# Performance work log

Measured on AMD Instinct MI355X. Metric: run time of the kernel, lower is better.

The kernel has to match this reference:

```python
import jax, jax.numpy as jnp
import numpy as np

NEG_SLOPE = 0.2  # DenseGATConv default negative_slope


def _add_self_loops(adj):
    n = adj.shape[-1]
    idx = jnp.arange(n)
    return adj.at[:, idx, idx].set(1.0)


def dense_gat_conv(x, adj, W, att_src, att_dst, bias, concat):
    """PyG DenseGATConv forward (eval mode, add_loop=True).
    x: [B,N,F], adj: [B,N,N] (0/1), W: [F,H*C], att_*: [H,C], bias: [H*C] or [C]."""
    B, N, _ = x.shape
    H, C = att_src.shape
    h = (x @ W).reshape(B, N, H, C)                     # projected features
    a_src = jnp.einsum('bnhc,hc->bnh', h, att_src)      # [B,N,H]
    a_dst = jnp.einsum('bnhc,hc->bnh', h, att_dst)      # [B,N,H]
    # alpha[b,i,j,h] = a_src[b,j,h] + a_dst[b,i,h]
    alpha = a_src[:, None, :, :] + a_dst[:, :, None, :]  # [B,N,N,H]
    alpha = jax.nn.leaky_relu(alpha, NEG_SLOPE)
    adj = _add_self_loops(adj)
    alpha = jnp.where(adj[..., None] == 0, -jnp.inf, alpha)
    alpha = jax.nn.softmax(alpha, axis=2)               # softmax over sources j
    out = jnp.einsum('bijh,bjhc->bihc', alpha, h)       # [B,N,H,C]
    out = out.reshape(B, N, H * C) if concat else out.mean(axis=2)
    return out + bias


def setup_inputs() -> dict:
    key = jax.random.key(0)
    ks = jax.random.split(key, 10)
    B, N, F, H, C, NC = 1, 4096, 512, 8, 64, 16
    x = jax.random.normal(ks[0], (B, N, F), dtype=jnp.float32)
    adj = (jax.random.uniform(ks[1], (B, N, N)) < 0.01).astype(jnp.float32)
    s1 = 1.0 / np.sqrt(F)
    s2 = 1.0 / np.sqrt(H * C)
    return {
        'x': x,
        'adj': adj,
        'W1': jax.random.normal(ks[2], (F, H * C), dtype=jnp.float32) * s1,
        'att_src1': jax.random.normal(ks[3], (H, C), dtype=jnp.float32) * s1,
        'att_dst1': jax.random.normal(ks[4], (H, C), dtype=jnp.float32) * s1,
        'b1': jnp.zeros((H * C,), dtype=jnp.float32),
        'W2': jax.random.normal(ks[5], (H * C, NC), dtype=jnp.float32) * s2,
        'att_src2': jax.random.normal(ks[6], (1, NC), dtype=jnp.float32) * s2,
        'att_dst2': jax.random.normal(ks[7], (1, NC), dtype=jnp.float32) * s2,
        'b2': jnp.zeros((NC,), dtype=jnp.float32),
    }


def reference(x, adj, W1, att_src1, att_dst1, b1, W2, att_src2, att_dst2, b2):
    # eval mode: all dropout(p=0.6) layers are identity
    h = dense_gat_conv(x, adj, W1, att_src1, att_dst1, b1, concat=True)
    h = jax.nn.elu(h)
    out = dense_gat_conv(h, adj, W2, att_src2, att_dst2, b2, concat=False)
    return out
```

## Files before the change

kernel.cpp:

```cpp
#include <hip/hip_runtime.h>
#include <hip/hip_bf16.h>
#include <hip/hip_fp16.h>

#define N_NODES 4096
#define F_IN    512
#define HC      512
#define H_HEADS 8
#define C_DIM   64
#define NCLS    16
#define CAP     192
#define NEG_SLOPE 0.2f

typedef __bf16 bf16x8 __attribute__((ext_vector_type(8)));
typedef float  f32x4  __attribute__((ext_vector_type(4)));
typedef unsigned short us8 __attribute__((ext_vector_type(8)));


#define XBLKS 1024
#define WBLKS 64

__global__ __launch_bounds__(256) void k_prep(const float* __restrict__ x,
                                              const float* __restrict__ W,
                                              const float* __restrict__ adj,
                                              ushort* __restrict__ xhi,
                                              ushort* __restrict__ xlo,
                                              ushort* __restrict__ whiT,
                                              ushort* __restrict__ wloT,
                                              int* __restrict__ row_cnt,
                                              int* __restrict__ col_idx) {
    __shared__ float tile[64][65];
    __shared__ int cnt_s;
    int b = blockIdx.x;
    int t = threadIdx.x;
    if (b < XBLKS) {
        int tid = b * 256 + t;
        int rg = tid >> 9;
        rg = tid >> 10;
        int c  = tid & 1023;
        int kb = c >> 6;
        int l  = c & 63;
        int row = rg * 16 + (l & 15);
        int kbase = kb * 32 + (l >> 4) * 8;
        const float* src = &x[(size_t)row * F_IN + kbase];
        float4 v0 = *(const float4*)&src[0];
        float4 v1 = *(const float4*)&src[4];
        float f[8] = {v0.x, v0.y, v0.z, v0.w, v1.x, v1.y, v1.z, v1.w};
        us8 hv, lv;
#pragma unroll
        for (int u = 0; u < 8; ++u) {
            __bf16 h = (__bf16)f[u];
            __bf16 lo_ = (__bf16)(f[u] - (float)h);
            hv[u] = __builtin_bit_cast(unsigned short, h);
            lv[u] = __builtin_bit_cast(unsigned short, lo_);
        }
        *(us8*)&xhi[(size_t)tid * 8] = hv;
        *(us8*)&xlo[(size_t)tid * 8] = lv;
    } else if (b < XBLKS + WBLKS) {
        int bb = b - XBLKS;
        int n0 = (bb & 7) * 64, k0 = (bb >> 3) * 64;
#pragma unroll
        for (int i = 0; i < 4; ++i) {
            int r = i * 16 + (t >> 4);
            int c = (t & 15) * 4;
            *(float4*)&tile[r][c] = *(const float4*)&W[(size_t)(k0 + r) * HC + n0 + c];
        }
        __syncthreads();
        int rg_local = t >> 6;
        int l = t & 63;
        int n_local = rg_local * 16 + (l & 15);
#pragma unroll
        for (int kb_local = 0; kb_local < 2; ++kb_local) {
            int k_local = kb_local * 32 + (l >> 4) * 8;
            us8 hv, lv;
#pragma unroll
            for (int u = 0; u < 8; ++u) {
                float f = tile[k_local + u][n_local];
                __bf16 h = (__bf16)f;
                __bf16 lo_ = (__bf16)(f - (float)h);
                hv[u] = __builtin_bit_cast(unsigned short, h);
                lv[u] = __builtin_bit_cast(unsigned short, lo_);
            }
            int rg = (n0 >> 4) + rg_local;
            int kb = (k0 >> 5) + kb_local;
            size_t off = ((size_t)(rg * 16 + kb) * 64 + l) * 8;
            *(us8*)&whiT[off] = hv;
            *(us8*)&wloT[off] = lv;
        }
    } else {
        int i = b - (XBLKS + WBLKS);
        if (t == 0) cnt_s = 0;
        __syncthreads();
        const float4* row = (const float4*)(adj + (size_t)i * N_NODES);
        int* cols = col_idx + (size_t)i * CAP;
#pragma unroll
        for (int it = 0; it < 4; ++it) {
            int idx4 = it * 256 + t;
            float4 v = row[idx4];
            int j0 = idx4 * 4;
            if (v.x != 0.f && j0 + 0 != i) { int p = atomicAdd(&cnt_s, 1); if (p < CAP - 1) cols[p] = j0 + 0; }
            if (v.y != 0.f && j0 + 1 != i) { int p = atomicAdd(&cnt_s, 1); if (p < CAP - 1) cols[p] = j0 + 1; }
            if (v.z != 0.f && j0 + 2 != i) { int p = atomicAdd(&cnt_s, 1); if (p < CAP - 1) cols[p] = j0 + 2; }
            if (v.w != 0.f && j0 + 3 != i) { int p = atomicAdd(&cnt_s, 1); if (p < CAP - 1) cols[p] = j0 + 3; }
        }
        __syncthreads();
        if (t == 0) {
            int p = min(cnt_s, CAP - 1);
            cols[p] = i;
            row_cnt[i] = p + 1;
        }
    }
}

__global__ __launch_bounds__(256) void k_gemm1(const ushort* __restrict__ Ahi,
                                               const ushort* __restrict__ Alo,
                                               const ushort* __restrict__ Bhi,
                                               const ushort* __restrict__ Blo,
                                               const float* __restrict__ att_src,
                                               const float* __restrict__ att_dst,
                                               __half* __restrict__ C,
                                               float* __restrict__ a_src,
                                               float* __restrict__ a_dst) {
    __shared__ __align__(16) ushort smem[4][2048];
    __shared__ float s_s[2][64], s_d[2][64];
    int t = threadIdx.x;
    int w = t >> 6, lane = t & 63;
    int n0 = blockIdx.x * 64;
    int m0 = blockIdx.y * 64;
    const ushort* src = (w == 0) ? Ahi : (w == 1) ? Alo : (w == 2) ? Bhi : Blo;
    int rg0 = ((w < 2) ? m0 : n0) >> 4;
    int mw = (w & 1) * 32, nw = (w >> 1) * 32;
    f32x4 acc[2][2] = {};
    for (int kb = 0; kb < 16; ++kb) {
#pragma unroll
        for (int g = 0; g < 4; ++g) {
            const ushort* gp = src + ((size_t)((rg0 + g) * 16 + kb) * 64 + lane) * 8;
            __builtin_amdgcn_global_load_lds(
                (const __attribute__((address_space(1))) void*)gp,
                (__attribute__((address_space(3))) void*)&smem[w][g * 512],
                16, 0, 0);
        }
        __syncthreads();
        bf16x8 ahi[2], alo[2], bhi[2], blo[2];
#pragma unroll
        for (int mi = 0; mi < 2; ++mi) {
            int g = (mw >> 4) + mi;
            ahi[mi] = __builtin_bit_cast(bf16x8, *(const us8*)&smem[0][g * 512 + lane * 8]);
            alo[mi] = __builtin_bit_cast(bf16x8, *(const us8*)&smem[1][g * 512 + lane * 8]);
        }
#pragma unroll
        for (int ni = 0; ni < 2; ++ni) {
            int g = (nw >> 4) + ni;
            bhi[ni] = __builtin_bit_cast(bf16x8, *(const us8*)&smem[2][g * 512 + lane * 8]);
            blo[ni] = __builtin_bit_cast(bf16x8, *(const us8*)&smem[3][g * 512 + lane * 8]);
        }
#pragma unroll
        for (int mi = 0; mi < 2; ++mi)
#pragma unroll
            for (int ni = 0; ni < 2; ++ni) {
                acc[mi][ni] = __builtin_amdgcn_mfma_f32_16x16x32_bf16(ahi[mi], bhi[ni], acc[mi][ni], 0, 0, 0);
                acc[mi][ni] = __builtin_amdgcn_mfma_f32_16x16x32_bf16(alo[mi], bhi[ni], acc[mi][ni], 0, 0, 0);
                acc[mi][ni] = __builtin_amdgcn_mfma_f32_16x16x32_bf16(ahi[mi], blo[ni], acc[mi][ni], 0, 0, 0);
            }
        __syncthreads();
    }
    int r0 = (lane >> 4) * 4;
    int cn = lane & 15;
    float as0 = att_src[n0 + nw + cn],      as1 = att_src[n0 + nw + 16 + cn];
    float ad0 = att_dst[n0 + nw + cn],      ad1 = att_dst[n0 + nw + 16 + cn];
#pragma unroll
    for (int mi = 0; mi < 2; ++mi)
#pragma unroll
        for (int r = 0; r < 4; ++r) {
            float ps = acc[mi][0][r] * as0 + acc[mi][1][r] * as1;
            float pd = acc[mi][0][r] * ad0 + acc[mi][1][r] * ad1;
#pragma unroll
            for (int o = 1; o < 16; o <<= 1) {
                ps += __shfl_xor(ps, o, 64);
                pd += __shfl_xor(pd, o, 64);
            }
            if (cn == 0) {
                int row = mw + mi * 16 + r0 + r;
                s_s[w >> 1][row] = ps;
                s_d[w >> 1][row] = pd;
            }
        }
#pragma unroll
    for (int mi = 0; mi < 2; ++mi)
#pragma unroll
        for (int ni = 0; ni < 2; ++ni) {
            size_t base = (size_t)(m0 + mw + mi * 16 + r0) * HC + (n0 + nw + ni * 16 + cn);
#pragma unroll
            for (int r = 0; r < 4; ++r)
                C[base + (size_t)r * HC] = __float2half(acc[mi][ni][r]);
        }
    __syncthreads();
    if (t < 64) {
        a_src[(m0 + t) * H_HEADS + blockIdx.x] = s_s[0][t] + s_s[1][t];
        a_dst[(m0 + t) * H_HEADS + blockIdx.x] = s_d[0][t] + s_d[1][t];
    }
}

__global__ __launch_bounds__(256) void k_agg1(const __half* __restrict__ hf,
                                              const float* __restrict__ a_src,
                                              const float* __restrict__ a_dst,
                                              const int* __restrict__ row_cnt,
                                              const int* __restrict__ col_idx,
                                              const float* __restrict__ b1,
                                              __half* __restrict__ elu1) {
    int i = blockIdx.x;
    int t = threadIdx.x;
    __shared__ float wL[CAP][H_HEADS];
    __shared__ int   colL[CAP];
    __shared__ float denom[H_HEADS];
    __shared__ float ad[H_HEADS];
    int cnt = row_cnt[i];
    if (t < H_HEADS) ad[t] = a_dst[i * H_HEADS + t];
    for (int j = t; j < cnt; j += 256) colL[j] = col_idx[(size_t)i * CAP + j];
    __syncthreads();
    for (int idx = t; idx < cnt * H_HEADS; idx += 256) {
        int j = idx >> 3, h = idx & 7;
        float l = a_src[colL[j] * H_HEADS + h] + ad[h];
        l = (l > 0.f) ? l : NEG_SLOPE * l;
        wL[j][h] = __expf(l);
    }
    __syncthreads();
    {
        int h = t >> 5, l32 = t & 31;
        float s = 0.f;
        for (int j = l32; j < cnt; j += 32) s += wL[j][h];
#pragma unroll
        for (int o = 16; o > 0; o >>= 1) s += __shfl_down(s, o, 32);
        if (l32 == 0) denom[h] = s;
    }
    __syncthreads();
    int e = t * 2;
    int h = e >> 6;
    float ax = 0.f, ay = 0.f;
    int j = 0;
    for (; j + 4 <= cnt; j += 4) {
        int c0 = colL[j], c1 = colL[j + 1], c2 = colL[j + 2], c3 = colL[j + 3];
        float2 v0 = __half22float2(*(const __half2*)&hf[(size_t)c0 * HC + e]);
        float2 v1 = __half22float2(*(const __half2*)&hf[(size_t)c1 * HC + e]);
        float2 v2 = __half22float2(*(const __half2*)&hf[(size_t)c2 * HC + e]);
        float2 v3 = __half22float2(*(const __half2*)&hf[(size_t)c3 * HC + e]);
        float w0 = wL[j][h], w1 = wL[j + 1][h], w2 = wL[j + 2][h], w3 = wL[j + 3][h];
        ax += w0 * v0.x + w1 * v1.x + w2 * v2.x + w3 * v3.x;
        ay += w0 * v0.y + w1 * v1.y + w2 * v2.y + w3 * v3.y;
    }
    for (; j < cnt; ++j) {
        int c0 = colL[j];
        float2 v0 = __half22float2(*(const __half2*)&hf[(size_t)c0 * HC + e]);
        float w0 = wL[j][h];
        ax += w0 * v0.x;
        ay += w0 * v0.y;
    }
    float inv = 1.f / denom[h];
    float o0 = ax * inv + b1[e];
    float o1 = ay * inv + b1[e + 1];
    o0 = (o0 > 0.f) ? o0 : (__expf(o0) - 1.f);
    o1 = (o1 > 0.f) ? o1 : (__expf(o1) - 1.f);
    *(__half2*)&elu1[(size_t)i * HC + e] = __floats2half2_rn(o0, o1);
}

__global__ __launch_bounds__(256) void k_gemm2(const __half* __restrict__ elu1,
                                               const float* __restrict__ W2,
                                               const float* __restrict__ att_src2,
                                               const float* __restrict__ att_dst2,
                                               float* __restrict__ h2,
                                               float* __restrict__ a_src2,
                                               float* __restrict__ a_dst2) {
    __shared__ float W2s[HC * NCLS];
    __shared__ float h2s[16][NCLS];
    int t = threadIdx.x;
    int n0 = blockIdx.x * 16;
#pragma unroll
    for (int u = 0; u < 8; ++u) {
        int idx = (u * 256 + t) * 4;
        *(float4*)&W2s[idx] = *(const float4*)&W2[idx];
    }
    __syncthreads();
    int nl = t >> 4, c = t & 15;
    const __half2* row = (const __half2*)(elu1 + (size_t)(n0 + nl) * HC);
    float acc = 0.f;
    for (int k = 0; k < HC; k += 4) {
        float2 v0 = __half22float2(row[k >> 1]);
        float2 v1 = __half22float2(row[(k >> 1) + 1]);
        acc += v0.x * W2s[(k + 0) * NCLS + c] + v0.y * W2s[(k + 1) * NCLS + c]
             + v1.x * W2s[(k + 2) * NCLS + c] + v1.y * W2s[(k + 3) * NCLS + c];
    }
    h2[(size_t)(n0 + nl) * NCLS + c] = acc;
    h2s[nl][c] = acc;
    __syncthreads();
    if (t < 16) {
        float s = 0.f, d = 0.f;
#pragma unroll
        for (int cc = 0; cc < NCLS; ++cc) {
            s += h2s[t][cc] * att_src2[cc];
            d += h2s[t][cc] * att_dst2[cc];
        }
        a_src2[n0 + t] = s;
        a_dst2[n0 + t] = d;
    }
}

__global__ __launch_bounds__(256) void k_agg2(const float* __restrict__ h2,
                                              const float* __restrict__ a_src2,
                                              const float* __restrict__ a_dst2,
                                              const int* __restrict__ row_cnt,
                                              const int* __restrict__ col_idx,
                                              const float* __restrict__ b2,
                                              float* __restrict__ out) {
    int t = threadIdx.x;
    int w = t >> 6, lane = t & 63;
    int i = blockIdx.x * 4 + w;
    __shared__ float ew[4][CAP];
    __shared__ int   colL[4][CAP];
    int cnt = row_cnt[i];
    float adi = a_dst2[i];
    float sum = 0.f;
    for (int j = lane; j < cnt; j += 64) {
        int col = col_idx[(size_t)i * CAP + j];
        colL[w][j] = col;
        float l = a_src2[col] + adi;
        l = (l > 0.f) ? l : NEG_SLOPE * l;
        float e = __expf(l);
        ew[w][j] = e;
        sum += e;
    }
#pragma unroll
    for (int o = 32; o > 0; o >>= 1) sum += __shfl_xor(sum, o, 64);
    int q = lane >> 4, c = lane & 15;
    float acc = 0.f;
    for (int j = q; j < cnt; j += 4)
        acc += ew[w][j] * h2[(size_t)colL[w][j] * NCLS + c];
    acc += __shfl_down(acc, 32, 64);
    acc += __shfl_down(acc, 16, 64);
    if (lane < NCLS)
        out[(size_t)i * NCLS + lane] = acc / sum + b2[lane];
}

extern "C" void kernel_launch(void* const* d_in, const int* in_sizes, int n_in,
                              void* d_out, int out_size, void* d_ws, size_t ws_size,
                              hipStream_t stream) {
    const float* x        = (const float*)d_in[0];
    const float* adj      = (const float*)d_in[1];
    const float* W1       = (const float*)d_in[2];
    const float* att_src1 = (const float*)d_in[3];
    const float* att_dst1 = (const float*)d_in[4];
    const float* b1       = (const float*)d_in[5];
    const float* W2       = (const float*)d_in[6];
    const float* att_src2 = (const float*)d_in[7];
    const float* att_dst2 = (const float*)d_in[8];
    const float* b2       = (const float*)d_in[9];
    float* out = (float*)d_out;

    char* ws = (char*)d_ws;
    int*    row_cnt = (int*)ws;     ws += (size_t)N_NODES * 4;
    int*    col_idx = (int*)ws;     ws += (size_t)N_NODES * CAP * 4;
    __half* h1f     = (__half*)ws;  ws += (size_t)N_NODES * HC * 2;
    float*  a_src   = (float*)ws;   ws += (size_t)N_NODES * H_HEADS * 4;
    float*  a_dst   = (float*)ws;   ws += (size_t)N_NODES * H_HEADS * 4;
    __half* elu1    = (__half*)ws;  ws += (size_t)N_NODES * HC * 2;
    float*  h2      = (float*)ws;   ws += (size_t)N_NODES * NCLS * 4;
    float*  as2     = (float*)ws;   ws += (size_t)N_NODES * 4;
    float*  ad2     = (float*)ws;   ws += (size_t)N_NODES * 4;
    ushort* x_hi    = (ushort*)ws;  ws += (size_t)N_NODES * F_IN * 2;
    ushort* x_lo    = (ushort*)ws;  ws += (size_t)N_NODES * F_IN * 2;
    ushort* w_hiT   = (ushort*)ws;  ws += (size_t)F_IN * HC * 2;
    ushort* w_loT   = (ushort*)ws;  ws += (size_t)F_IN * HC * 2;

    hipLaunchKernelGGL(k_prep, dim3(XBLKS + WBLKS + N_NODES), dim3(256), 0, stream,
                       x, W1, adj, x_hi, x_lo, w_hiT, w_loT, row_cnt, col_idx);
    hipLaunchKernelGGL(k_gemm1, dim3(HC / 64, N_NODES / 64), dim3(256), 0, stream,
                       x_hi, x_lo, w_hiT, w_loT, att_src1, att_dst1, h1f, a_src, a_dst);
    hipLaunchKernelGGL(k_agg1, dim3(N_NODES), dim3(256), 0, stream,
                       h1f, a_src, a_dst, row_cnt, col_idx, b1, elu1);
    hipLaunchKernelGGL(k_gemm2, dim3(N_NODES / 16), dim3(256), 0, stream,
                       elu1, W2, att_src2, att_dst2, h2, as2, ad2);
    hipLaunchKernelGGL(k_agg2, dim3(N_NODES / 4), dim3(256), 0, stream,
                       h2, as2, ad2, row_cnt, col_idx, b2, out);
}
```

Measured before the change: 165.2 us.

## Fuse second-layer projection into layer-1 aggregation kernel

The layer-1 aggregation kernel now keeps each row's ELU output in shared memory and immediately multiplies it by W2, also computing the layer-2 attention scores. This removes the separate gemm2 launch and the fp16 ELU intermediate's write and re-read. The cost is that every one of 4096 blocks reloads the full 32 KB W2 into shared memory, and the larger shared footprint may reduce occupancy. It also adds extra block barriers and a serial tail per row.

```diff
diff --git a/kernel.cpp b/kernel.cpp
--- a/kernel.cpp
+++ b/kernel.cpp
@@ -34,8 +34,7 @@
     int t = threadIdx.x;
     if (b < XBLKS) {
         int tid = b * 256 + t;
-        int rg = tid >> 9;
-        rg = tid >> 10;
+        int rg = tid >> 10;
         int c  = tid & 1023;
         int kb = c >> 6;
         int l  = c & 63;
@@ -206,16 +205,30 @@
                                               const int* __restrict__ row_cnt,
                                               const int* __restrict__ col_idx,
                                               const float* __restrict__ b1,
-                                              __half* __restrict__ elu1) {
+                                              const float* __restrict__ W2,
+                                              const float* __restrict__ att_src2,
+                                              const float* __restrict__ att_dst2,
+                                              float* __restrict__ h2,
+                                              float* __restrict__ a_src2,
+                                              float* __restrict__ a_dst2) {
     int i = blockIdx.x;
     int t = threadIdx.x;
     __shared__ float wL[CAP][H_HEADS];
     __shared__ int   colL[CAP];
     __shared__ float denom[H_HEADS];
     __shared__ float ad[H_HEADS];
+    __shared__ float W2s[HC * NCLS];
+    __shared__ float elu_s[HC];
+    __shared__ float part[16][NCLS + 1];
+    __shared__ float h2row[NCLS];
     int cnt = row_cnt[i];
     if (t < H_HEADS) ad[t] = a_dst[i * H_HEADS + t];
     for (int j = t; j < cnt; j += 256) colL[j] = col_idx[(size_t)i * CAP + j];
+#pragma unroll
+    for (int u = 0; u < 8; ++u) {
+        int idx = (u * 256 + t) * 4;
+        *(float4*)&W2s[idx] = *(const float4*)&W2[idx];
+    }
     __syncthreads();
     for (int idx = t; idx < cnt * H_HEADS; idx += 256) {
         int j = idx >> 3, h = idx & 7;
@@ -259,47 +272,37 @@
     float o1 = ay * inv + b1[e + 1];
     o0 = (o0 > 0.f) ? o0 : (__expf(o0) - 1.f);
     o1 = (o1 > 0.f) ? o1 : (__expf(o1) - 1.f);
-    *(__half2*)&elu1[(size_t)i * HC + e] = __floats2half2_rn(o0, o1);
-}
-
-__global__ __launch_bounds__(256) void k_gemm2(const __half* __restrict__ elu1,
-                                               const float* __restrict__ W2,
-                                               const float* __restrict__ att_src2,
-                                               const float* __restrict__ att_dst2,
-                                               float* __restrict__ h2,
-                                               float* __restrict__ a_src2,
-                                               float* __restrict__ a_dst2) {
-    __shared__ float W2s[HC * NCLS];
-    __shared__ float h2s[16][NCLS];
-    int t = threadIdx.x;
-    int n0 = blockIdx.x * 16;
-#pragma unroll
-    for (int u = 0; u < 8; ++u) {
-        int idx = (u * 256 + t) * 4;
-        *(float4*)&W2s[idx] = *(const float4*)&W2[idx];
-    }
-    __syncthreads();
-    int nl = t >> 4, c = t & 15;
-    const __half2* row = (const __half2*)(elu1 + (size_t)(n0 + nl) * HC);
-    float acc = 0.f;
-    for (int k = 0; k < HC; k += 4) {
-        float2 v0 = __half22float2(row[k >> 1]);
-        float2 v1 = __half22float2(row[(k >> 1) + 1]);
-        acc += v0.x * W2s[(k + 0) * NCLS + c] + v0.y * W2s[(k + 1) * NCLS + c]
-             + v1.x * W2s[(k + 2) * NCLS + c] + v1.y * W2s[(k + 3) * NCLS + c];
-    }
-    h2[(size_t)(n0 + nl) * NCLS + c] = acc;
-    h2s[nl][c] = acc;
-    __syncthreads();
-    if (t < 16) {
+    elu_s[e] = o0;
+    elu_s[e + 1] = o1;
+    __syncthreads();
+    {
+        int p = t >> 4, c = t & 15;
+        float acc2 = 0.f;
+#pragma unroll 8
+        for (int ks = 0; ks < 32; ++ks) {
+            int k = p * 32 + ks;
+            acc2 += elu_s[k] * W2s[k * NCLS + c];
+        }
+        part[p][c] = acc2;
+    }
+    __syncthreads();
+    if (t < NCLS) {
+        float v = 0.f;
+#pragma unroll
+        for (int pp = 0; pp < 16; ++pp) v += part[pp][t];
+        h2[(size_t)i * NCLS + t] = v;
+        h2row[t] = v;
+    }
+    __syncthreads();
+    if (t == 0) {
         float s = 0.f, d = 0.f;
 #pragma unroll
         for (int cc = 0; cc < NCLS; ++cc) {
-            s += h2s[t][cc] * att_src2[cc];
-            d += h2s[t][cc] * att_dst2[cc];
-        }
-        a_src2[n0 + t] = s;
-        a_dst2[n0 + t] = d;
+            s += h2row[cc] * att_src2[cc];
+            d += h2row[cc] * att_dst2[cc];
+        }
+        a_src2[i] = s;
+        a_dst2[i] = d;
     }
 }
 
@@ -360,7 +363,6 @@
     __half* h1f     = (__half*)ws;  ws += (size_t)N_NODES * HC * 2;
     float*  a_src   = (float*)ws;   ws += (size_t)N_NODES * H_HEADS * 4;
     float*  a_dst   = (float*)ws;   ws += (size_t)N_NODES * H_HEADS * 4;
-    __half* elu1    = (__half*)ws;  ws += (size_t)N_NODES * HC * 2;
     float*  h2      = (float*)ws;   ws += (size_t)N_NODES * NCLS * 4;
     float*  as2     = (float*)ws;   ws += (size_t)N_NODES * 4;
     float*  ad2     = (float*)ws;   ws += (size_t)N_NODES * 4;
@@ -374,9 +376,8 @@
     hipLaunchKernelGGL(k_gemm1, dim3(HC / 64, N_NODES / 64), dim3(256), 0, stream,
                        x_hi, x_lo, w_hiT, w_loT, att_src1, att_dst1, h1f, a_src, a_dst);
     hipLaunchKernelGGL(k_agg1, dim3(N_NODES), dim3(256), 0, stream,
-                       h1f, a_src, a_dst, row_cnt, col_idx, b1, elu1);
-    hipLaunchKernelGGL(k_gemm2, dim3(N_NODES / 16), dim3(256), 0, stream,
-                       elu1, W2, att_src2, att_dst2, h2, as2, ad2);
+                       h1f, a_src, a_dst, row_cnt, col_idx, b1, W2, att_src2, att_dst2,
+                       h2, as2, ad2);
     hipLaunchKernelGGL(k_agg2, dim3(N_NODES / 4), dim3(256), 0, stream,
                        h2, as2, ad2, row_cnt, col_idx, b2, out);
 }
```

New measurement: 177.6 us. 1.08x slower.

## Split layer-1 aggregation across four wavefronts with 16-byte gathers and LDS reduction

Applied to the files above, without the earlier changes.

The layer-1 neighbor aggregation used to have each thread read a 4-byte half2 slice of every neighbor row. Now each of the four 64-lane wavefronts takes every fourth neighbor, and each lane loads 8 halves (16 bytes) per row. The four partial sums go into shared memory and are added before normalization, bias and ELU. The aim is wider, more coalesced gathers and more memory parallelism, at the cost of an extra 8 KB of LDS and more registers per thread. It also removes a redundant assignment in the prep kernel.

```diff
diff --git a/kernel.cpp b/kernel.cpp
--- a/kernel.cpp
+++ b/kernel.cpp
@@ -34,8 +34,7 @@
     int t = threadIdx.x;
     if (b < XBLKS) {
         int tid = b * 256 + t;
-        int rg = tid >> 9;
-        rg = tid >> 10;
+        int rg = tid >> 10;
         int c  = tid & 1023;
         int kb = c >> 6;
         int l  = c & 63;
@@ -213,6 +212,7 @@
     __shared__ int   colL[CAP];
     __shared__ float denom[H_HEADS];
     __shared__ float ad[H_HEADS];
+    __shared__ float part[4][HC];
     int cnt = row_cnt[i];
     if (t < H_HEADS) ad[t] = a_dst[i * H_HEADS + t];
     for (int j = t; j < cnt; j += 256) colL[j] = col_idx[(size_t)i * CAP + j];
@@ -232,28 +232,45 @@
         for (int o = 16; o > 0; o >>= 1) s += __shfl_down(s, o, 32);
         if (l32 == 0) denom[h] = s;
     }
+    int g = t >> 6, lane = t & 63;
+    int c0 = lane * 8;
+    int hh = lane >> 3;
+    float acc[8] = {};
+    int j = g;
+    for (; j + 8 <= cnt; j += 8) {
+        int colA = colL[j], colB = colL[j + 4];
+        float4 vA = *(const float4*)&hf[(size_t)colA * HC + c0];
+        float4 vB = *(const float4*)&hf[(size_t)colB * HC + c0];
+        float wA = wL[j][hh], wB = wL[j + 4][hh];
+        __half2* hA = (__half2*)&vA;
+        __half2* hB = (__half2*)&vB;
+#pragma unroll
+        for (int u = 0; u < 4; ++u) {
+            float2 pA = __half22float2(hA[u]);
+            float2 pB = __half22float2(hB[u]);
+            acc[2 * u]     += wA * pA.x + wB * pB.x;
+            acc[2 * u + 1] += wA * pA.y + wB * pB.y;
+        }
+    }
+    for (; j < cnt; j += 4) {
+        int col = colL[j];
+        float4 v = *(const float4*)&hf[(size_t)col * HC + c0];
+        float wj = wL[j][hh];
+        __half2* hp = (__half2*)&v;
+#pragma unroll
+        for (int u = 0; u < 4; ++u) {
+            float2 p = __half22float2(hp[u]);
+            acc[2 * u]     += wj * p.x;
+            acc[2 * u + 1] += wj * p.y;
+        }
+    }
+    *(float4*)&part[g][c0]     = make_float4(acc[0], acc[1], acc[2], acc[3]);
+    *(float4*)&part[g][c0 + 4] = make_float4(acc[4], acc[5], acc[6], acc[7]);
     __syncthreads();
     int e = t * 2;
     int h = e >> 6;
-    float ax = 0.f, ay = 0.f;
-    int j = 0;
-    for (; j + 4 <= cnt; j += 4) {
-        int c0 = colL[j], c1 = colL[j + 1], c2 = colL[j + 2], c3 = colL[j + 3];
-        float2 v0 = __half22float2(*(const __half2*)&hf[(size_t)c0 * HC + e]);
-        float2 v1 = __half22float2(*(const __half2*)&hf[(size_t)c1 * HC + e]);
-        float2 v2 = __half22float2(*(const __half2*)&hf[(size_t)c2 * HC + e]);
-        float2 v3 = __half22float2(*(const __half2*)&hf[(size_t)c3 * HC + e]);
-        float w0 = wL[j][h], w1 = wL[j + 1][h], w2 = wL[j + 2][h], w3 = wL[j + 3][h];
-        ax += w0 * v0.x + w1 * v1.x + w2 * v2.x + w3 * v3.x;
-        ay += w0 * v0.y + w1 * v1.y + w2 * v2.y + w3 * v3.y;
-    }
-    for (; j < cnt; ++j) {
-        int c0 = colL[j];
-        float2 v0 = __half22float2(*(const __half2*)&hf[(size_t)c0 * HC + e]);
-        float w0 = wL[j][h];
-        ax += w0 * v0.x;
-        ay += w0 * v0.y;
-    }
+    float ax = part[0][e] + part[1][e] + part[2][e] + part[3][e];
+    float ay = part[0][e + 1] + part[1][e + 1] + part[2][e + 1] + part[3][e + 1];
     float inv = 1.f / denom[h];
     float o0 = ax * inv + b1[e];
     float o1 = ay * inv + b1[e + 1];
```

Measured after the change: 167.7 us. About the same (+1.5%).
